# Performance work log

Hardware: AMD Instinct MI355X
Metric: run time of the kernel (lower is better)

The kernel has to match this reference:

```python
import jax, jax.numpy as jnp
import numpy as np

N, S, D_IN, D, H, L, DFF, NRBF = 3072, 256, 64, 256, 8, 3, 1024, 8
LN_EPS = 1e-5
RBF_C = jnp.linspace(0.0, 1.0, NRBF)
RBF_W = jnp.full((NRBF,), 0.15)


def _ln(x, g, b):
    m = x.mean(-1, keepdims=True)
    v = ((x - m) ** 2).mean(-1, keepdims=True)
    return (x - m) * jax.lax.rsqrt(v + LN_EPS) * g + b


def _rbf(v):
    return jnp.exp(-0.5 * ((v[..., None] - RBF_C) / (RBF_W + 1e-6)) ** 2)


def _mha(Q, K, V, Win, bin_, Wout, bout, bias, pad):
    # manual biased MHA: [Lq,D],[Lk,D] -> [Lq,D]; bias [Lq,Lk], pad [Lk] bool
    d = D // H
    q = (Q @ Win[:D].T + bin_[:D]).reshape(-1, H, d).transpose(1, 0, 2)        # [H,Lq,d]
    k = (K @ Win[D:2 * D].T + bin_[D:2 * D]).reshape(-1, H, d).transpose(1, 0, 2)
    v = (V @ Win[2 * D:].T + bin_[2 * D:]).reshape(-1, H, d).transpose(1, 0, 2)
    scores = jnp.einsum('hqd,hkd->hqk', q, k) / (d ** 0.5)
    scores = scores + bias[None]
    scores = scores - 10000.0 * pad.astype(scores.dtype)[None, None, :]
    scores = scores - scores.max(-1, keepdims=True)
    scores = jnp.clip(scores, -20.0, 20.0)
    attn = jax.nn.softmax(scores, axis=-1)
    out = jnp.einsum('hqk,hkd->hqd', attn, v).transpose(1, 0, 2).reshape(-1, D)
    return out @ Wout.T + bout


def _ff(x, W1, b1, W2, b2):
    return jax.nn.gelu(x @ W1.T + b1, approximate=False) @ W2.T + b2


def _forward(x, C, proj_in_W, proj_in_b, pe_W, pe_b, pe_g, pe_beta, pe_gate,
             alpha_nn, beta_sn, sq_W, sq_b,
             sn_Win, sn_bin, sn_Wout, sn_bout, nn_Win, nn_bin, nn_Wout, nn_bout,
             ln_s_g, ln_s_b, ln_n1_g, ln_n1_b, ln_n2_g, ln_n2_b,
             ffn_W1, ffn_b1, ffn_W2, ffn_b2, ffs_W1, ffs_b1, ffs_W2, ffs_b2,
             ln_out_g, ln_out_b, sink_idx, mask_nodes):
    h = x @ proj_in_W.T + proj_in_b                                            # [N,D]
    # correlation-aware node encoding
    Cc = jnp.clip(C, 0.0, 1.0)
    cm, cmax, cmin, cstd = Cc.mean(-1), Cc.max(-1), Cc.min(-1), Cc.std(-1)
    z = jnp.concatenate([cm[:, None], cmax[:, None], cmin[:, None], cstd[:, None],
                         _rbf(cm), _rbf(cmax)], axis=-1)                       # [N,4+2*NRBF]
    pe = pe_gate * _ln(z @ pe_W.T + pe_b, pe_g, pe_beta)
    pe = jnp.where(mask_nodes[:, None], 0.0, pe)
    h = h + pe
    # sink queries (detached gather, then projection)
    sink_q = jax.lax.stop_gradient(h[sink_idx]) @ sq_W.T + sq_b                # [S,D]
    # correlation-derived attention biases
    Cn = C / (jnp.linalg.norm(C, axis=-1, keepdims=True) + 1e-6)
    bias_nn = alpha_nn * (Cn @ Cn.T)                                           # [N,N]
    bias_sn = beta_sn * C.T                                                    # [S,N]
    for l in range(L):
        sq_res = sink_q
        sqn = _ln(sink_q, ln_s_g[l], ln_s_b[l])
        sink_q = sq_res + _mha(sqn, h, h, sn_Win[l], sn_bin[l], sn_Wout[l], sn_bout[l], bias_sn, mask_nodes)
        sink_q = sink_q + _ff(sink_q, ffs_W1[l], ffs_b1[l], ffs_W2[l], ffs_b2[l])
        h_res = h
        hn = _ln(h, ln_n1_g[l], ln_n1_b[l])
        h = h_res + _mha(hn, hn, hn, nn_Win[l], nn_bin[l], nn_Wout[l], nn_bout[l], bias_nn, mask_nodes)
        h = h + _ff(_ln(h, ln_n2_g[l], ln_n2_b[l]), ffn_W1[l], ffn_b1[l], ffn_W2[l], ffn_b2[l])
    return _ln(sink_q, ln_out_g, ln_out_b)                                     # [S,D]


def setup_inputs() -> dict:
    key = jax.random.key(0)
    ks = iter(jax.random.split(key, 48))
    def nrm(shape, s=0.02):
        return jax.random.normal(next(ks), shape, jnp.float32) * s
    FEAT = 4 + 2 * NRBF
    return dict(
        x=jax.random.normal(next(ks), (N, D_IN), jnp.float32),
        C=jax.random.uniform(next(ks), (N, S), jnp.float32),
        sink_idx=jax.random.randint(next(ks), (S,), 0, N),
        mask_nodes=jnp.zeros((N,), bool),
        proj_in_W=nrm((D, D_IN)), proj_in_b=nrm((D,)),
        pe_W=nrm((D, FEAT)), pe_b=nrm((D,)),
        pe_g=jnp.ones((D,)), pe_beta=jnp.zeros((D,)),
        pe_gate=jnp.asarray(0.1, jnp.float32),
        alpha_nn=jnp.asarray(0.3, jnp.float32), beta_sn=jnp.asarray(0.8, jnp.float32),
        sq_W=nrm((D, D)), sq_b=nrm((D,)),
        sn_Win=nrm((L, 3 * D, D)), sn_bin=nrm((L, 3 * D)), sn_Wout=nrm((L, D, D)), sn_bout=nrm((L, D)),
        nn_Win=nrm((L, 3 * D, D)), nn_bin=nrm((L, 3 * D)), nn_Wout=nrm((L, D, D)), nn_bout=nrm((L, D)),
        ln_s_g=jnp.ones((L, D)), ln_s_b=jnp.zeros((L, D)),
        ln_n1_g=jnp.ones((L, D)), ln_n1_b=jnp.zeros((L, D)),
        ln_n2_g=jnp.ones((L, D)), ln_n2_b=jnp.zeros((L, D)),
        ffn_W1=nrm((L, DFF, D)), ffn_b1=nrm((L, DFF)), ffn_W2=nrm((L, D, DFF)), ffn_b2=nrm((L, D)),
        ffs_W1=nrm((L, DFF, D)), ffs_b1=nrm((L, DFF)), ffs_W2=nrm((L, D, DFF)), ffs_b2=nrm((L, D)),
        ln_out_g=jnp.ones((D,)), ln_out_b=jnp.zeros((D,)),
    )


def reference(x, C, sink_idx, mask_nodes, proj_in_W, proj_in_b, pe_W, pe_b, pe_g, pe_beta, pe_gate,
              alpha_nn, beta_sn, sq_W, sq_b,
              sn_Win, sn_bin, sn_Wout, sn_bout, nn_Win, nn_bin, nn_Wout, nn_bout,
              ln_s_g, ln_s_b, ln_n1_g, ln_n1_b, ln_n2_g, ln_n2_b,
              ffn_W1, ffn_b1, ffn_W2, ffn_b2, ffs_W1, ffs_b1, ffs_W2, ffs_b2,
              ln_out_g, ln_out_b):
    return _forward(x, C, proj_in_W, proj_in_b, pe_W, pe_b, pe_g, pe_beta, pe_gate,
                    alpha_nn, beta_sn, sq_W, sq_b,
                    sn_Win, sn_bin, sn_Wout, sn_bout, nn_Win, nn_bin, nn_Wout, nn_bout,
                    ln_s_g, ln_s_b, ln_n1_g, ln_n1_b, ln_n2_g, ln_n2_b,
                    ffn_W1, ffn_b1, ffn_W2, ffn_b2, ffs_W1, ffs_b1, ffs_W2, ffs_b2,
                    ln_out_g, ln_out_b, sink_idx, mask_nodes)
```

## Files before the change

kernel.cpp:

```cpp
#include <hip/hip_runtime.h>
#include <hip/hip_bf16.h>

#define N_NODES 3072
#define S_SINK  256
#define DIN     64
#define NH      8

typedef __attribute__((ext_vector_type(8))) short short8v;
typedef __attribute__((ext_vector_type(4))) float f32x4;

#define LOG2E 1.4426950408889634f

#if defined(__has_builtin)
#if __has_builtin(__builtin_amdgcn_exp2f)
#define EXP2(x) __builtin_amdgcn_exp2f(x)
#else
#define EXP2(x) exp2f(x)
#endif
#else
#define EXP2(x) exp2f(x)
#endif

static __device__ __forceinline__ float gelu_exact(float v) {
    return 0.5f * v * (1.0f + erff(v * 0.70710678118654752f));
}
static __device__ __forceinline__ unsigned short f2b_rne(float f) {
    unsigned int b = __float_as_uint(f);
    b += 0x7fffu + ((b >> 16) & 1u);
    return (unsigned short)(b >> 16);
}
static __device__ __forceinline__ unsigned pack_b16(float a, float b) {
    unsigned r;
    asm("v_cvt_pk_bf16_f32 %0, %1, %2" : "=v"(r) : "v"(a), "v"(b));
    return r;
}
static __device__ __forceinline__ size_t bswz_idx(int m, int n) {
    int qt = m >> 4, cc = m & 15;
    int kt = n >> 4, gg = (n >> 2) & 3, rr = n & 3;
    return (((size_t)qt * 192 + kt) * 64 + gg * 16 + cc) * 4 + rr;
}
static __device__ __forceinline__ size_t kfrag_idx(int h, int k, int d) {
    return (((size_t)(h * 192 + (k >> 4)) * 64) + ((d >> 3) << 4) + (k & 15)) * 8 + (d & 7);
}
static __device__ __forceinline__ size_t vtfrag_idx(int h, int k, int d) {
    return ((((size_t)(h * 48 + (k >> 6)) * 2 + ((k >> 5) & 1)) * 2 + (d >> 4)) * 64
            + ((k >> 3) & 3) * 16 + (d & 15)) * 8 + (k & 7);
}

struct CvtJobs {
    const float* src[9];
    unsigned short* dst[9];
    int cnt4[9];
};
__global__ __launch_bounds__(256) void prep_misc_kernel(CvtJobs cj, int total4, int ncvt,
                                                        const unsigned char* __restrict__ mask,
                                                        float* __restrict__ ma,
                                                        const float* __restrict__ C,
                                                        unsigned short* __restrict__ Cnb)
{
    int b = blockIdx.x;
    if (b < ncvt) {
        int i = b * 256 + threadIdx.x;
        if (i >= total4) return;
        int s = 0, base = 0;
        while (s < 9 && i >= base + cj.cnt4[s]) { base += cj.cnt4[s]; ++s; }
        int off = (i - base) * 4;
        float4 v = *(const float4*)(cj.src[s] + off);
        uint2 o;
        o.x = pack_b16(v.x, v.y);
        o.y = pack_b16(v.z, v.w);
        *(uint2*)(cj.dst[s] + off) = o;
        return;
    }
    b -= ncvt;
    if (b < 12) {
        int j = b * 256 + threadIdx.x;
        if (j < N_NODES) ma[j] = -10000.0f * LOG2E * (float)mask[j];
        return;
    }
    b -= 12;
    int w = threadIdx.x >> 6, lane = threadIdx.x & 63;
    int row = b * 4 + w;
    float4 v = *(const float4*)(C + (size_t)row * 256 + lane * 4);
    float s2 = v.x * v.x + v.y * v.y + v.z * v.z + v.w * v.w;
    #pragma unroll
    for (int o = 32; o > 0; o >>= 1) s2 += __shfl_xor(s2, o);
    float inv = 1.0f / (sqrtf(s2) + 1e-6f);
    uint2 o2;
    o2.x = pack_b16(v.x * inv, v.y * inv);
    o2.y = pack_b16(v.z * inv, v.w * inv);
    *(uint2*)(Cnb + (size_t)row * 256 + lane * 4) = o2;
}

__global__ __launch_bounds__(256) void node_encode_kernel(
    const float* __restrict__ x, const float* __restrict__ C,
    const unsigned char* __restrict__ mask,
    const float* __restrict__ Wp, const float* __restrict__ bp,
    const float* __restrict__ peW, const float* __restrict__ peb,
    const float* __restrict__ peg, const float* __restrict__ pebt,
    const float* __restrict__ gate,
    float* __restrict__ h, unsigned short* __restrict__ hb)
{
    int i = blockIdx.x, t = threadIdx.x;
    __shared__ float xs[DIN];
    __shared__ float r1[256], r2[256];
    __shared__ float zs[20];
    if (t < DIN) xs[t] = x[i * DIN + t];
    float c  = C[i * 256 + t];
    float cc = fminf(fmaxf(c, 0.0f), 1.0f);
    r1[t] = cc; r2[t] = cc * cc;
    __syncthreads();
    for (int s = 128; s > 0; s >>= 1) { if (t < s) { r1[t] += r1[t + s]; r2[t] += r2[t + s]; } __syncthreads(); }
    float cm  = r1[0] * (1.0f / 256.0f);
    float cms = r2[0] * (1.0f / 256.0f);
    __syncthreads();
    r1[t] = cc; r2[t] = cc;
    __syncthreads();
    for (int s = 128; s > 0; s >>= 1) { if (t < s) { r1[t] = fmaxf(r1[t], r1[t + s]); r2[t] = fminf(r2[t], r2[t + s]); } __syncthreads(); }
    float cmax = r1[0], cmin = r2[0];
    __syncthreads();
    if (t == 0) {
        float var  = fmaxf(cms - cm * cm, 0.0f);
        float cstd = sqrtf(var);
        zs[0] = cm; zs[1] = cmax; zs[2] = cmin; zs[3] = cstd;
        float w = 0.15f + 1e-6f;
        for (int k = 0; k < 8; ++k) {
            float ck = (float)k / 7.0f;
            float d1 = (cm   - ck) / w;
            float d2 = (cmax - ck) / w;
            zs[4 + k]  = expf(-0.5f * d1 * d1);
            zs[12 + k] = expf(-0.5f * d2 * d2);
        }
    }
    __syncthreads();
    float pl = peb[t];
    #pragma unroll
    for (int f = 0; f < 20; ++f) pl += zs[f] * peW[t * 20 + f];
    r1[t] = pl; r2[t] = pl * pl;
    __syncthreads();
    for (int s = 128; s > 0; s >>= 1) { if (t < s) { r1[t] += r1[t + s]; r2[t] += r2[t + s]; } __syncthreads(); }
    float m  = r1[0] * (1.0f / 256.0f);
    float vv = fmaxf(r2[0] * (1.0f / 256.0f) - m * m, 0.0f);
    float pe = (pl - m) * rsqrtf(vv + 1e-5f) * peg[t] + pebt[t];
    pe *= gate[0];
    if (mask[i] != 0) pe = 0.0f;
    float hv = bp[t];
    #pragma unroll
    for (int k = 0; k < DIN; ++k) hv += xs[k] * Wp[t * DIN + k];
    float o = hv + pe;
    h[(size_t)i * 256 + t] = o;
    hb[(size_t)i * 256 + t] = f2b_rne(o);
}

static __device__ __forceinline__ void ln_row(const float* in, const float* g, const float* b,
                                              unsigned short* out, int row, int lane) {
    float4 v = *(const float4*)(in + (size_t)row * 256 + lane * 4);
    float s  = v.x + v.y + v.z + v.w;
    float s2 = v.x * v.x + v.y * v.y + v.z * v.z + v.w * v.w;
    #pragma unroll
    for (int o = 32; o > 0; o >>= 1) { s += __shfl_xor(s, o); s2 += __shfl_xor(s2, o); }
    float m  = s * (1.0f / 256.0f);
    float vv = fmaxf(s2 * (1.0f / 256.0f) - m * m, 0.0f);
    float rs = rsqrtf(vv + 1e-5f);
    float4 gg = *(const float4*)(g + lane * 4);
    float4 bb = *(const float4*)(b + lane * 4);
    uint2 o2;
    o2.x = pack_b16((v.x - m) * rs * gg.x + bb.x, (v.y - m) * rs * gg.y + bb.y);
    o2.y = pack_b16((v.z - m) * rs * gg.z + bb.z, (v.w - m) * rs * gg.w + bb.w);
    *(uint2*)(out + (size_t)row * 256 + lane * 4) = o2;
}

__global__ __launch_bounds__(256) void ln_b16_w_kernel(const float* __restrict__ in, const float* __restrict__ g,
                                                       const float* __restrict__ b, unsigned short* __restrict__ out) {
    int w = threadIdx.x >> 6, lane = threadIdx.x & 63;
    ln_row(in, g, b, out, blockIdx.x * 4 + w, lane);
}

__global__ __launch_bounds__(256) void ln_dual_kernel(const float* __restrict__ in0, const float* __restrict__ g0,
                                                      const float* __restrict__ b0, unsigned short* __restrict__ out0, int n0,
                                                      const float* __restrict__ in1, const float* __restrict__ g1,
                                                      const float* __restrict__ b1, unsigned short* __restrict__ out1) {
    int w = threadIdx.x >> 6, lane = threadIdx.x & 63;
    int row = blockIdx.x * 4 + w;
    bool first = row < n0;
    const float* in = first ? in0 : in1;
    const float* g  = first ? g0  : g1;
    const float* b  = first ? b0  : b1;
    unsigned short* out = first ? out0 : out1;
    ln_row(in, g, b, out, first ? row : row - n0, lane);
}

__global__ __launch_bounds__(256) void ln_out_w_kernel(const float* __restrict__ in, const float* __restrict__ g,
                                                       const float* __restrict__ b, float* __restrict__ out) {
    int w = threadIdx.x >> 6, lane = threadIdx.x & 63;
    int row = blockIdx.x * 4 + w;
    float4 v = *(const float4*)(in + (size_t)row * 256 + lane * 4);
    float s  = v.x + v.y + v.z + v.w;
    float s2 = v.x * v.x + v.y * v.y + v.z * v.z + v.w * v.w;
    #pragma unroll
    for (int o = 32; o > 0; o >>= 1) { s += __shfl_xor(s, o); s2 += __shfl_xor(s2, o); }
    float m  = s * (1.0f / 256.0f);
    float vv = fmaxf(s2 * (1.0f / 256.0f) - m * m, 0.0f);
    float rs = rsqrtf(vv + 1e-5f);
    float4 gg = *(const float4*)(g + lane * 4);
    float4 bb = *(const float4*)(b + lane * 4);
    float4 o4;
    o4.x = (v.x - m) * rs * gg.x + bb.x;
    o4.y = (v.y - m) * rs * gg.y + bb.y;
    o4.z = (v.z - m) * rs * gg.z + bb.z;
    o4.w = (v.w - m) * rs * gg.w + bb.w;
    *(float4*)(out + (size_t)row * 256 + lane * 4) = o4;
}

struct GJob {
    const unsigned short* A; const int* ridx; const unsigned short* W;
    const float* bias; const float* res; const float* scale;
    void* out; void* out2; void* vtf;
    int lda, ldw, ldo, omode, kbase, K, act, gx;
    float scmul;
};

static __device__ __forceinline__ void gemm_body(const GJob& j, int bx, int by) {
    __shared__ unsigned short As[64][72];
    __shared__ unsigned short Ws[64][72];
    int tid = threadIdx.x;
    int lane = tid & 63, wid = tid >> 6;
    int c15 = lane & 15, g = lane >> 4;
    int wm = wid & 1, wn = wid >> 1;
    int row0 = by * 64, col0 = bx * 64;
    f32x4 acc[2][2];
    const f32x4 zf = {0.f, 0.f, 0.f, 0.f};
    acc[0][0] = zf; acc[0][1] = zf; acc[1][0] = zf; acc[1][1] = zf;

    for (int k0 = 0; k0 < j.K; k0 += 64) {
        #pragma unroll
        for (int hh = 0; hh < 2; ++hh) {
            int cid = tid + hh * 256;
            int rr = cid >> 3, cc = (cid & 7) * 8;
            int arow = j.ridx ? j.ridx[row0 + rr] : (row0 + rr);
            short8v va = *(const short8v*)(j.A + (size_t)arow * j.lda + k0 + cc);
            short8v vw = *(const short8v*)(j.W + (size_t)(col0 + rr) * j.ldw + k0 + cc);
            *(short8v*)(&As[rr][cc]) = va;
            *(short8v*)(&Ws[rr][cc]) = vw;
        }
        __syncthreads();
        #pragma unroll
        for (int ks = 0; ks < 2; ++ks) {
            short8v a0 = *(const short8v*)(&As[wm * 32 + c15][ks * 32 + g * 8]);
            short8v a1 = *(const short8v*)(&As[wm * 32 + 16 + c15][ks * 32 + g * 8]);
            short8v w0 = *(const short8v*)(&Ws[wn * 32 + c15][ks * 32 + g * 8]);
            short8v w1 = *(const short8v*)(&Ws[wn * 32 + 16 + c15][ks * 32 + g * 8]);
            acc[0][0] = __builtin_amdgcn_mfma_f32_16x16x32_bf16(a0, w0, acc[0][0], 0, 0, 0);
            acc[0][1] = __builtin_amdgcn_mfma_f32_16x16x32_bf16(a0, w1, acc[0][1], 0, 0, 0);
            acc[1][0] = __builtin_amdgcn_mfma_f32_16x16x32_bf16(a1, w0, acc[1][0], 0, 0, 0);
            acc[1][1] = __builtin_amdgcn_mfma_f32_16x16x32_bf16(a1, w1, acc[1][1], 0, 0, 0);
        }
        __syncthreads();
    }
    float sc = (j.scale ? *j.scale : 1.0f) * j.scmul;
    #pragma unroll
    for (int nf = 0; nf < 2; ++nf) {
        int n = col0 + wn * 32 + nf * 16 + c15;
        float bv = j.bias ? j.bias[n] : 0.0f;
        #pragma unroll
        for (int mf = 0; mf < 2; ++mf) {
            #pragma unroll
            for (int r = 0; r < 4; ++r) {
                int m = row0 + wm * 32 + mf * 16 + g * 4 + r;
                float v = acc[mf][nf][r] * sc + bv;
                if (j.act) v = gelu_exact(v);
                if (j.res) v += j.res[(size_t)m * j.ldo + n];
                if (j.omode == 0) {
                    ((float*)j.out)[(size_t)m * j.ldo + n] = v;
                    if (j.out2) ((unsigned short*)j.out2)[(size_t)m * j.ldo + n] = f2b_rne(v);
                } else if (j.omode == 1) {
                    ((unsigned short*)j.out)[(size_t)m * j.ldo + n] = f2b_rne(v);
                } else if (j.omode == 2) {
                    ((unsigned short*)j.out)[bswz_idx(m, n)] = f2b_rne(v);
                } else {
                    unsigned short bw = f2b_rne(v);
                    int nk = n - j.kbase;
                    if (nk < 0) {
                        ((unsigned short*)j.out)[(size_t)m * j.ldo + n] = bw;
                    } else if (nk < 256) {
                        ((unsigned short*)j.out2)[kfrag_idx(nk >> 5, m, nk & 31)] = bw;
                    } else {
                        ((unsigned short*)j.vtf)[vtfrag_idx((nk - 256) >> 5, m, (nk - 256) & 31)] = bw;
                    }
                }
            }
        }
    }
}

__global__ __launch_bounds__(256) void gemm_multi_kernel(GJob j0, GJob j1, GJob j2, int e0, int e1) {
    int b = blockIdx.x;
    GJob j;
    int bb;
    if (b < e0)      { j = j0; bb = b; }
    else if (b < e1) { j = j1; bb = b - e0; }
    else             { j = j2; bb = b - e1; }
    gemm_body(j, bb % j.gx, bb / j.gx);
}

static __device__ __forceinline__ void transpose_body(const float* C, const float* beta,
                                                      const float* maskadd, unsigned short* CTswz,
                                                      int bxi, int byi) {
    __shared__ float tile[32][33];
    int bx = bxi * 32;
    int by = byi * 32;
    int tx = threadIdx.x & 31, ty = threadIdx.x >> 5;
    float bt = beta[0] * LOG2E;
    #pragma unroll
    for (int r = 0; r < 4; ++r) {
        int row = bx + ty + r * 8;
        tile[ty + r * 8][tx] = C[(size_t)row * 256 + by + tx];
    }
    __syncthreads();
    #pragma unroll
    for (int r = 0; r < 4; ++r) {
        int srow = by + ty + r * 8;
        int col  = bx + tx;
        CTswz[bswz_idx(srow, col)] = f2b_rne(bt * tile[tx][ty + r * 8] + maskadd[col]);
    }
}

__global__ __launch_bounds__(256) void mega0_kernel(
    const float* __restrict__ C, const float* __restrict__ beta,
    const float* __restrict__ maskadd, unsigned short* __restrict__ CTswz,
    GJob j0, GJob j1, int ntr, int e0)
{
    int b = blockIdx.x;
    if (b < ntr) { transpose_body(C, beta, maskadd, CTswz, b % 96, b / 96); return; }
    b -= ntr;
    GJob j;
    int bb;
    if (b < e0) { j = j0; bb = b; }
    else        { j = j1; bb = b - e0; }
    gemm_body(j, bb % j.gx, bb / j.gx);
}

template<int SPLIT>
static __device__ __forceinline__ void attn_body(
    const unsigned short* __restrict__ Qb, int ldq,
    const unsigned short* __restrict__ Kfrag,
    const unsigned short* __restrict__ VTfrag,
    const unsigned short* __restrict__ biasswz,
    unsigned short* __restrict__ out, int qx)
{
    constexpr int KT = 48 / SPLIT;
    __shared__ unsigned short P_all[SPLIT * 32 * 72];
    __shared__ float ml[SPLIT * 64];
    const int head = blockIdx.y;
    const int i0 = qx * 32;
    const int qt0 = qx * 2;
    const int tid = threadIdx.x;
    const int lane = tid & 63, w = tid >> 6;
    const int c15 = lane & 15, g = lane >> 4;
    unsigned short* P_lds = P_all + w * (32 * 72);
    const unsigned short* Kf  = Kfrag  + (size_t)head * 192 * 512;
    const unsigned short* VTf = VTfrag + (size_t)head * 48 * 2048;
    const f32x4 zf = {0.f, 0.f, 0.f, 0.f};
    const float rsl2 = 0.25503164113124427f;

    short8v qf[2];
    #pragma unroll
    for (int nf = 0; nf < 2; ++nf)
        qf[nf] = *(const short8v*)(Qb + (size_t)(i0 + nf * 16 + c15) * ldq + head * 32 + g * 8);

    float m_[2] = {-1e30f, -1e30f};
    float l_[2] = {0.f, 0.f};
    f32x4 acc[2][2];
    acc[0][0] = zf; acc[0][1] = zf; acc[1][0] = zf; acc[1][1] = zf;

    for (int kt = 0; kt < KT; ++kt) {
        const int k0 = (w * KT + kt) * 64;
        const int kt16 = k0 >> 4;
        short8v kf[4];
        #pragma unroll
        for (int mf = 0; mf < 4; ++mf)
            kf[mf] = *(const short8v*)(Kf + ((size_t)(kt16 + mf) * 64 + lane) * 8);
        f32x4 s[4][2];
        __builtin_amdgcn_s_setprio(1);
        #pragma unroll
        for (int mf = 0; mf < 4; ++mf)
            #pragma unroll
            for (int nf = 0; nf < 2; ++nf)
                s[mf][nf] = __builtin_amdgcn_mfma_f32_16x16x32_bf16(kf[mf], qf[nf], zf, 0, 0, 0);
        __builtin_amdgcn_s_setprio(0);
        #pragma unroll
        for (int nf = 0; nf < 2; ++nf) {
            const unsigned short* bb = biasswz + ((size_t)(qt0 + nf) * 192 + kt16) * 256 + lane * 4;
            #pragma unroll
            for (int mf = 0; mf < 4; ++mf) {
                uint2 bv = *(const uint2*)(bb + mf * 256);
                s[mf][nf][0] = s[mf][nf][0] * rsl2 + __uint_as_float(bv.x << 16);
                s[mf][nf][1] = s[mf][nf][1] * rsl2 + __uint_as_float(bv.x & 0xffff0000u);
                s[mf][nf][2] = s[mf][nf][2] * rsl2 + __uint_as_float(bv.y << 16);
                s[mf][nf][3] = s[mf][nf][3] * rsl2 + __uint_as_float(bv.y & 0xffff0000u);
            }
        }
        #pragma unroll
        for (int nf = 0; nf < 2; ++nf) {
            float t0 = fmaxf(fmaxf(s[0][nf][0], s[0][nf][1]), fmaxf(s[0][nf][2], s[0][nf][3]));
            float t1 = fmaxf(fmaxf(s[1][nf][0], s[1][nf][1]), fmaxf(s[1][nf][2], s[1][nf][3]));
            float t2 = fmaxf(fmaxf(s[2][nf][0], s[2][nf][1]), fmaxf(s[2][nf][2], s[2][nf][3]));
            float t3 = fmaxf(fmaxf(s[3][nf][0], s[3][nf][1]), fmaxf(s[3][nf][2], s[3][nf][3]));
            float tmax = fmaxf(fmaxf(t0, t1), fmaxf(t2, t3));
            tmax = fmaxf(tmax, __shfl_xor(tmax, 16));
            tmax = fmaxf(tmax, __shfl_xor(tmax, 32));
            if (!__all(tmax <= m_[nf] + 8.0f)) {
                float mn = fmaxf(m_[nf], tmax);
                float scl = EXP2(m_[nf] - mn);
                m_[nf] = mn;
                l_[nf] *= scl;
                #pragma unroll
                for (int mf = 0; mf < 2; ++mf) {
                    acc[mf][nf][0] *= scl; acc[mf][nf][1] *= scl;
                    acc[mf][nf][2] *= scl; acc[mf][nf][3] *= scl;
                }
            }
            float mcur = m_[nf];
            float ps0 = 0.f, ps1 = 0.f, ps2 = 0.f, ps3 = 0.f;
            #pragma unroll
            for (int mf = 0; mf < 4; ++mf) {
                float p0 = EXP2(s[mf][nf][0] - mcur);
                float p1 = EXP2(s[mf][nf][1] - mcur);
                float p2 = EXP2(s[mf][nf][2] - mcur);
                float p3 = EXP2(s[mf][nf][3] - mcur);
                s[mf][nf][0] = p0; s[mf][nf][1] = p1;
                s[mf][nf][2] = p2; s[mf][nf][3] = p3;
                ps0 += p0; ps1 += p1; ps2 += p2; ps3 += p3;
            }
            l_[nf] += (ps0 + ps1) + (ps2 + ps3);
            const int q = nf * 16 + c15;
            #pragma unroll
            for (int mf = 0; mf < 4; ++mf) {
                uint2 pv;
                pv.x = pack_b16(s[mf][nf][0], s[mf][nf][1]);
                pv.y = pack_b16(s[mf][nf][2], s[mf][nf][3]);
                *(uint2*)(P_lds + q * 72 + mf * 16 + g * 4) = pv;
            }
        }
        const unsigned short* vb = VTf + (size_t)(k0 >> 6) * 2048;
        #pragma unroll
        for (int ks = 0; ks < 2; ++ks) {
            short8v pB[2], vA[2];
            #pragma unroll
            for (int nf = 0; nf < 2; ++nf)
                pB[nf] = *(const short8v*)(P_lds + (nf * 16 + c15) * 72 + ks * 32 + g * 8);
            #pragma unroll
            for (int mf = 0; mf < 2; ++mf)
                vA[mf] = *(const short8v*)(vb + ((size_t)(ks * 2 + mf) * 64 + lane) * 8);
            __builtin_amdgcn_s_setprio(1);
            #pragma unroll
            for (int mf = 0; mf < 2; ++mf)
                #pragma unroll
                for (int nf = 0; nf < 2; ++nf)
                    acc[mf][nf] = __builtin_amdgcn_mfma_f32_16x16x32_bf16(vA[mf], pB[nf], acc[mf][nf], 0, 0, 0);
            __builtin_amdgcn_s_setprio(0);
        }
    }

    float* Olds = (float*)P_all;
    #pragma unroll
    for (int nf = 0; nf < 2; ++nf) {
        float lv = l_[nf];
        lv += __shfl_xor(lv, 16);
        lv += __shfl_xor(lv, 32);
        int q = nf * 16 + c15;
        #pragma unroll
        for (int mf = 0; mf < 2; ++mf)
            *(f32x4*)(Olds + w * 1152 + q * 36 + mf * 16 + g * 4) = acc[mf][nf];
        if (g == 0) {
            ml[w * 64 + q] = m_[nf];
            ml[w * 64 + 32 + q] = lv;
        }
    }
    __syncthreads();
    if (tid < 256) {
        int q = tid >> 3, d0 = (tid & 7) * 4;
        float M = -1e30f;
        #pragma unroll
        for (int s = 0; s < SPLIT; ++s) M = fmaxf(M, ml[s * 64 + q]);
        float L = 0.f;
        float v0 = 0, v1 = 0, v2 = 0, v3 = 0;
        #pragma unroll
        for (int s = 0; s < SPLIT; ++s) {
            float wv = EXP2(ml[s * 64 + q] - M);
            L += wv * ml[s * 64 + 32 + q];
            const float* op = Olds + s * 1152 + q * 36 + d0;
            v0 += wv * op[0]; v1 += wv * op[1];
            v2 += wv * op[2]; v3 += wv * op[3];
        }
        float invL = 1.0f / L;
        uint2 pk;
        pk.x = pack_b16(v0 * invL, v1 * invL);
        pk.y = pack_b16(v2 * invL, v3 * invL);
        *(uint2*)(out + (size_t)(i0 + q) * 256 + head * 32 + d0) = pk;
    }
}

template<int SPLIT>
__global__ __launch_bounds__(64 * SPLIT) void attn_multi_kernel(
    const unsigned short* Q0, const unsigned short* K0, const unsigned short* V0,
    const unsigned short* B0, unsigned short* O0, int nx0,
    const unsigned short* Q1, const unsigned short* K1, const unsigned short* V1,
    const unsigned short* B1, unsigned short* O1)
{
    int bx = blockIdx.x;
    bool first = bx < nx0;
    const unsigned short* Q = first ? Q0 : Q1;
    const unsigned short* K = first ? K0 : K1;
    const unsigned short* V = first ? V0 : V1;
    const unsigned short* B = first ? B0 : B1;
    unsigned short* O = first ? O0 : O1;
    attn_body<SPLIT>(Q, 256, K, V, B, O, first ? bx : bx - nx0);
}

extern "C" void kernel_launch(void* const* d_in, const int* in_sizes, int n_in,
                              void* d_out, int out_size, void* d_ws, size_t ws_size,
                              hipStream_t stream)
{
    const float* x        = (const float*)d_in[0];
    const float* C        = (const float*)d_in[1];
    const int*   sidx     = (const int*)d_in[2];
    const unsigned char* mask = (const unsigned char*)d_in[3];
    const float* proj_W   = (const float*)d_in[4];
    const float* proj_b   = (const float*)d_in[5];
    const float* peW      = (const float*)d_in[6];
    const float* peb      = (const float*)d_in[7];
    const float* peg      = (const float*)d_in[8];
    const float* pebt     = (const float*)d_in[9];
    const float* pe_gate  = (const float*)d_in[10];
    const float* alpha_nn = (const float*)d_in[11];
    const float* beta_sn  = (const float*)d_in[12];
    const float* sqW      = (const float*)d_in[13];
    const float* sqb      = (const float*)d_in[14];
    const float* sn_Win   = (const float*)d_in[15];
    const float* sn_bin   = (const float*)d_in[16];
    const float* sn_Wout  = (const float*)d_in[17];
    const float* sn_bout  = (const float*)d_in[18];
    const float* nn_Win   = (const float*)d_in[19];
    const float* nn_bin   = (const float*)d_in[20];
    const float* nn_Wout  = (const float*)d_in[21];
    const float* nn_bout  = (const float*)d_in[22];
    const float* ln_s_g   = (const float*)d_in[23];
    const float* ln_s_b   = (const float*)d_in[24];
    const float* ln_n1_g  = (const float*)d_in[25];
    const float* ln_n1_b  = (const float*)d_in[26];
    const float* ln_n2_g  = (const float*)d_in[27];
    const float* ln_n2_b  = (const float*)d_in[28];
    const float* ffn_W1   = (const float*)d_in[29];
    const float* ffn_b1   = (const float*)d_in[30];
    const float* ffn_W2   = (const float*)d_in[31];
    const float* ffn_b2   = (const float*)d_in[32];
    const float* ffs_W1   = (const float*)d_in[33];
    const float* ffs_b1   = (const float*)d_in[34];
    const float* ffs_W2   = (const float*)d_in[35];
    const float* ffs_b2   = (const float*)d_in[36];
    const float* ln_og    = (const float*)d_in[37];
    const float* ln_ob    = (const float*)d_in[38];

    float* ws = (float*)d_ws;
    float* h       = ws;
    float* sinkq   = ws + 786432;
    float* maskadd = ws + 851968;
    unsigned short* Cnb     = (unsigned short*)(ws + 856064);
    unsigned short* hb      = (unsigned short*)(ws + 1249280);
    unsigned short* hnb     = (unsigned short*)(ws + 1642496);
    unsigned short* attnob_n= (unsigned short*)(ws + 2035712);
    unsigned short* attnob_s= (unsigned short*)(ws + 2428928);
    unsigned short* sqnb    = (unsigned short*)(ws + 2461696);
    unsigned short* sinkqb  = (unsigned short*)(ws + 2494464);
    unsigned short* Kfrag_n = (unsigned short*)(ws + 2527232);
    unsigned short* VTfrag_n= (unsigned short*)(ws + 2920448);
    unsigned short* Kfrag_s = (unsigned short*)(ws + 3313664);
    unsigned short* VTfrag_s= (unsigned short*)(ws + 3706880);
    unsigned short* CTswz   = (unsigned short*)(ws + 4100096);
    unsigned short* biasswz = (unsigned short*)(ws + 4493312);
    unsigned short* wb      = (unsigned short*)(ws + 9211904);
    float* big      = ws + 11603968;
    unsigned short* sqWb    = wb;
    unsigned short* snWinb  = wb + 65536;
    unsigned short* snWoutb = wb + 655360;
    unsigned short* nnWinb  = wb + 851968;
    unsigned short* nnWoutb = wb + 1441792;
    unsigned short* ffnW1b  = wb + 1638400;
    unsigned short* ffnW2b  = wb + 2424832;
    unsigned short* ffsW1b  = wb + 3211264;
    unsigned short* ffsW2b  = wb + 3997696;
    unsigned short* q_sb  = (unsigned short*)big;
    unsigned short* mid_sb= (unsigned short*)big + 65536;
    unsigned short* Qnb   = (unsigned short*)big + 327680;
    unsigned short* midb  = (unsigned short*)big + 1114112;

    dim3 b256(256), b512(512);
    GJob jz = {};  jz.gx = 1;

    CvtJobs cj;
    cj.src[0] = sqW;     cj.dst[0] = sqWb;    cj.cnt4[0] = 16384;
    cj.src[1] = sn_Win;  cj.dst[1] = snWinb;  cj.cnt4[1] = 147456;
    cj.src[2] = sn_Wout; cj.dst[2] = snWoutb; cj.cnt4[2] = 49152;
    cj.src[3] = nn_Win;  cj.dst[3] = nnWinb;  cj.cnt4[3] = 147456;
    cj.src[4] = nn_Wout; cj.dst[4] = nnWoutb; cj.cnt4[4] = 49152;
    cj.src[5] = ffn_W1;  cj.dst[5] = ffnW1b;  cj.cnt4[5] = 196608;
    cj.src[6] = ffn_W2;  cj.dst[6] = ffnW2b;  cj.cnt4[6] = 196608;
    cj.src[7] = ffs_W1;  cj.dst[7] = ffsW1b;  cj.cnt4[7] = 196608;
    cj.src[8] = ffs_W2;  cj.dst[8] = ffsW2b;  cj.cnt4[8] = 196608;

    prep_misc_kernel<<<4672 + 12 + 768, b256, 0, stream>>>(cj, 1196032, 4672, mask, maskadd, C, Cnb);
    node_encode_kernel<<<N_NODES, b256, 0, stream>>>(x, C, mask, proj_W, proj_b, peW, peb, peg, pebt, pe_gate, h, hb);
    {
        GJob j0 = {hb, sidx, sqWb, sqb, nullptr, nullptr, sinkq, nullptr, nullptr, 256, 256, 256, 0, 0, 256, 0, 4, 1.0f};
        GJob j1 = {Cnb, nullptr, Cnb, maskadd, nullptr, alpha_nn, biasswz, nullptr, nullptr, 256, 256, 3072, 2, 0, 256, 0, 48, LOG2E};
        mega0_kernel<<<768 + 16 + 2304, b256, 0, stream>>>(C, beta_sn, maskadd, CTswz, j0, j1, 768, 16);
    }

    for (int l = 0; l < 3; ++l) {
        const float* lsg = ln_s_g + l * 256,  *lsb = ln_s_b + l * 256;
        const float* l1g = ln_n1_g + l * 256, *l1b = ln_n1_b + l * 256;
        ln_dual_kernel<<<832, b256, 0, stream>>>(sinkq, lsg, lsb, sqnb, 256, h, l1g, l1b, hnb);
        {
            GJob j0 = {sqnb, nullptr, snWinb + (size_t)l * 196608, sn_bin + l * 768, nullptr, nullptr, q_sb, nullptr, nullptr, 256, 256, 256, 1, 0, 256, 0, 4, 1.0f};
            GJob j1 = {hb, nullptr, snWinb + (size_t)l * 196608 + 65536, sn_bin + l * 768 + 256, nullptr, nullptr, nullptr, Kfrag_s, VTfrag_s, 256, 256, 0, 3, 0, 256, 0, 8, 1.0f};
            GJob j2 = {hnb, nullptr, nnWinb + (size_t)l * 196608, nn_bin + l * 768, nullptr, nullptr, Qnb, Kfrag_n, VTfrag_n, 256, 256, 256, 3, 256, 256, 0, 12, 1.0f};
            gemm_multi_kernel<<<16 + 384 + 576, b256, 0, stream>>>(j0, j1, j2, 16, 16 + 384);
        }
        attn_multi_kernel<8><<<dim3(8 + 96, 8), b512, 0, stream>>>(
            q_sb, Kfrag_s, VTfrag_s, CTswz, attnob_s, 8,
            Qnb, Kfrag_n, VTfrag_n, biasswz, attnob_n);
        {
            GJob j0 = {attnob_s, nullptr, snWoutb + (size_t)l * 65536, sn_bout + l * 256, sinkq, nullptr, sinkq, sinkqb, nullptr, 256, 256, 256, 0, 0, 256, 0, 4, 1.0f};
            GJob j1 = {attnob_n, nullptr, nnWoutb + (size_t)l * 65536, nn_bout + l * 256, h, nullptr, h, nullptr, nullptr, 256, 256, 256, 0, 0, 256, 0, 4, 1.0f};
            gemm_multi_kernel<<<16 + 192, b256, 0, stream>>>(j0, j1, jz, 16, 16 + 192);
        }
        ln_b16_w_kernel<<<768, b256, 0, stream>>>(h, ln_n2_g + l * 256, ln_n2_b + l * 256, hnb);
        {
            GJob j0 = {sinkqb, nullptr, ffsW1b + (size_t)l * 262144, ffs_b1 + l * 1024, nullptr, nullptr, mid_sb, nullptr, nullptr, 256, 256, 1024, 1, 0, 256, 1, 16, 1.0f};
            GJob j1 = {hnb, nullptr, ffnW1b + (size_t)l * 262144, ffn_b1 + l * 1024, nullptr, nullptr, midb, nullptr, nullptr, 256, 256, 1024, 1, 0, 256, 1, 16, 1.0f};
            gemm_multi_kernel<<<64 + 768, b256, 0, stream>>>(j0, j1, jz, 64, 64 + 768);
        }
        {
            GJob j0 = {mid_sb, nullptr, ffsW2b + (size_t)l * 262144, ffs_b2 + l * 256, sinkq, nullptr, sinkq, nullptr, nullptr, 1024, 1024, 256, 0, 0, 1024, 0, 4, 1.0f};
            GJob j1 = {midb, nullptr, ffnW2b + (size_t)l * 262144, ffn_b2 + l * 256, h, nullptr, h, hb, nullptr, 1024, 1024, 256, 0, 0, 1024, 0, 4, 1.0f};
            gemm_multi_kernel<<<16 + 192, b256, 0, stream>>>(j0, j1, jz, 16, 16 + 192);
        }
    }

    ln_out_w_kernel<<<64, b256, 0, stream>>>(sinkq, ln_og, ln_ob, (float*)d_out);
}
```

Measured before the change: 341.2 us.

## Fuse LayerNorm into GEMM A-tile load, drop standalone LN kernels

Removes the separate ln_dual and ln_b16 kernels. The GEMM now takes the fp32 pre-norm activations plus gamma and beta. Each block first computes per-row mean and rstd into shared memory, then normalizes and converts to bf16 while staging the A tile. This saves two kernel launches per layer and the bf16 normalized-activation round trip through memory. In exchange, every column tile recomputes the row statistics and reads fp32 A, which is twice the bytes of bf16, across all N-tiles (12 or 16 column blocks).

Result: slower. 440.7 us (+29.1%).

```diff
diff --git a/kernel.cpp b/kernel.cpp
--- a/kernel.cpp
+++ b/kernel.cpp
@@ -152,44 +152,6 @@
     hb[(size_t)i * 256 + t] = f2b_rne(o);
 }
 
-static __device__ __forceinline__ void ln_row(const float* in, const float* g, const float* b,
-                                              unsigned short* out, int row, int lane) {
-    float4 v = *(const float4*)(in + (size_t)row * 256 + lane * 4);
-    float s  = v.x + v.y + v.z + v.w;
-    float s2 = v.x * v.x + v.y * v.y + v.z * v.z + v.w * v.w;
-    #pragma unroll
-    for (int o = 32; o > 0; o >>= 1) { s += __shfl_xor(s, o); s2 += __shfl_xor(s2, o); }
-    float m  = s * (1.0f / 256.0f);
-    float vv = fmaxf(s2 * (1.0f / 256.0f) - m * m, 0.0f);
-    float rs = rsqrtf(vv + 1e-5f);
-    float4 gg = *(const float4*)(g + lane * 4);
-    float4 bb = *(const float4*)(b + lane * 4);
-    uint2 o2;
-    o2.x = pack_b16((v.x - m) * rs * gg.x + bb.x, (v.y - m) * rs * gg.y + bb.y);
-    o2.y = pack_b16((v.z - m) * rs * gg.z + bb.z, (v.w - m) * rs * gg.w + bb.w);
-    *(uint2*)(out + (size_t)row * 256 + lane * 4) = o2;
-}
-
-__global__ __launch_bounds__(256) void ln_b16_w_kernel(const float* __restrict__ in, const float* __restrict__ g,
-                                                       const float* __restrict__ b, unsigned short* __restrict__ out) {
-    int w = threadIdx.x >> 6, lane = threadIdx.x & 63;
-    ln_row(in, g, b, out, blockIdx.x * 4 + w, lane);
-}
-
-__global__ __launch_bounds__(256) void ln_dual_kernel(const float* __restrict__ in0, const float* __restrict__ g0,
-                                                      const float* __restrict__ b0, unsigned short* __restrict__ out0, int n0,
-                                                      const float* __restrict__ in1, const float* __restrict__ g1,
-                                                      const float* __restrict__ b1, unsigned short* __restrict__ out1) {
-    int w = threadIdx.x >> 6, lane = threadIdx.x & 63;
-    int row = blockIdx.x * 4 + w;
-    bool first = row < n0;
-    const float* in = first ? in0 : in1;
-    const float* g  = first ? g0  : g1;
-    const float* b  = first ? b0  : b1;
-    unsigned short* out = first ? out0 : out1;
-    ln_row(in, g, b, out, first ? row : row - n0, lane);
-}
-
 __global__ __launch_bounds__(256) void ln_out_w_kernel(const float* __restrict__ in, const float* __restrict__ g,
                                                        const float* __restrict__ b, float* __restrict__ out) {
     int w = threadIdx.x >> 6, lane = threadIdx.x & 63;
@@ -216,6 +178,7 @@
     const unsigned short* A; const int* ridx; const unsigned short* W;
     const float* bias; const float* res; const float* scale;
     void* out; void* out2; void* vtf;
+    const float* lnA; const float* lng; const float* lnb;
     int lda, ldw, ldo, omode, kbase, K, act, gx;
     float scmul;
 };
@@ -223,6 +186,7 @@
 static __device__ __forceinline__ void gemm_body(const GJob& j, int bx, int by) {
     __shared__ unsigned short As[64][72];
     __shared__ unsigned short Ws[64][72];
+    __shared__ float lnm[64], lnr[64];
     int tid = threadIdx.x;
     int lane = tid & 63, wid = tid >> 6;
     int c15 = lane & 15, g = lane >> 4;
@@ -232,16 +196,54 @@
     const f32x4 zf = {0.f, 0.f, 0.f, 0.f};
     acc[0][0] = zf; acc[0][1] = zf; acc[1][0] = zf; acc[1][1] = zf;
 
+    if (j.lnA) {
+        int r = tid >> 2, p = tid & 3;
+        int arow = j.ridx ? j.ridx[row0 + r] : (row0 + r);
+        const float* src = j.lnA + (size_t)arow * j.lda + p * 64;
+        float s = 0.f, s2 = 0.f;
+        #pragma unroll
+        for (int i = 0; i < 16; ++i) {
+            float4 v = *(const float4*)(src + i * 4);
+            s  += (v.x + v.y) + (v.z + v.w);
+            s2 += (v.x * v.x + v.y * v.y) + (v.z * v.z + v.w * v.w);
+        }
+        s  += __shfl_xor(s, 1);  s2 += __shfl_xor(s2, 1);
+        s  += __shfl_xor(s, 2);  s2 += __shfl_xor(s2, 2);
+        if (p == 0) {
+            float m = s * (1.0f / 256.0f);
+            float vv = fmaxf(s2 * (1.0f / 256.0f) - m * m, 0.0f);
+            lnm[r] = m;
+            lnr[r] = rsqrtf(vv + 1e-5f);
+        }
+        __syncthreads();
+    }
+
     for (int k0 = 0; k0 < j.K; k0 += 64) {
         #pragma unroll
         for (int hh = 0; hh < 2; ++hh) {
             int cid = tid + hh * 256;
             int rr = cid >> 3, cc = (cid & 7) * 8;
             int arow = j.ridx ? j.ridx[row0 + rr] : (row0 + rr);
-            short8v va = *(const short8v*)(j.A + (size_t)arow * j.lda + k0 + cc);
-            short8v vw = *(const short8v*)(j.W + (size_t)(col0 + rr) * j.ldw + k0 + cc);
-            *(short8v*)(&As[rr][cc]) = va;
-            *(short8v*)(&Ws[rr][cc]) = vw;
+            if (j.lnA) {
+                const float* p4 = j.lnA + (size_t)arow * j.lda + k0 + cc;
+                float m = lnm[rr], rs = lnr[rr];
+                float4 a0 = *(const float4*)p4;
+                float4 a1 = *(const float4*)(p4 + 4);
+                float4 g0 = *(const float4*)(j.lng + k0 + cc);
+                float4 g1 = *(const float4*)(j.lng + k0 + cc + 4);
+                float4 b0 = *(const float4*)(j.lnb + k0 + cc);
+                float4 b1 = *(const float4*)(j.lnb + k0 + cc + 4);
+                uint2 lo, hi;
+                lo.x = pack_b16((a0.x - m) * rs * g0.x + b0.x, (a0.y - m) * rs * g0.y + b0.y);
+                lo.y = pack_b16((a0.z - m) * rs * g0.z + b0.z, (a0.w - m) * rs * g0.w + b0.w);
+                hi.x = pack_b16((a1.x - m) * rs * g1.x + b1.x, (a1.y - m) * rs * g1.y + b1.y);
+                hi.y = pack_b16((a1.z - m) * rs * g1.z + b1.z, (a1.w - m) * rs * g1.w + b1.w);
+                *(uint2*)(&As[rr][cc]) = lo;
+                *(uint2*)(&As[rr][cc + 4]) = hi;
+            } else {
+                *(short8v*)(&As[rr][cc]) = *(const short8v*)(j.A + (size_t)arow * j.lda + k0 + cc);
+            }
+            *(short8v*)(&Ws[rr][cc]) = *(const short8v*)(j.W + (size_t)(col0 + rr) * j.ldw + k0 + cc);
         }
         __syncthreads();
         #pragma unroll
@@ -568,10 +570,8 @@
     float* maskadd = ws + 851968;
     unsigned short* Cnb     = (unsigned short*)(ws + 856064);
     unsigned short* hb      = (unsigned short*)(ws + 1249280);
-    unsigned short* hnb     = (unsigned short*)(ws + 1642496);
     unsigned short* attnob_n= (unsigned short*)(ws + 2035712);
     unsigned short* attnob_s= (unsigned short*)(ws + 2428928);
-    unsigned short* sqnb    = (unsigned short*)(ws + 2461696);
     unsigned short* sinkqb  = (unsigned short*)(ws + 2494464);
     unsigned short* Kfrag_n = (unsigned short*)(ws + 2527232);
     unsigned short* VTfrag_n= (unsigned short*)(ws + 2920448);
@@ -612,38 +612,48 @@
     prep_misc_kernel<<<4672 + 12 + 768, b256, 0, stream>>>(cj, 1196032, 4672, mask, maskadd, C, Cnb);
     node_encode_kernel<<<N_NODES, b256, 0, stream>>>(x, C, mask, proj_W, proj_b, peW, peb, peg, pebt, pe_gate, h, hb);
     {
-        GJob j0 = {hb, sidx, sqWb, sqb, nullptr, nullptr, sinkq, nullptr, nullptr, 256, 256, 256, 0, 0, 256, 0, 4, 1.0f};
-        GJob j1 = {Cnb, nullptr, Cnb, maskadd, nullptr, alpha_nn, biasswz, nullptr, nullptr, 256, 256, 3072, 2, 0, 256, 0, 48, LOG2E};
+        GJob j0 = {hb, sidx, sqWb, sqb, nullptr, nullptr, sinkq, nullptr, nullptr,
+                   nullptr, nullptr, nullptr, 256, 256, 256, 0, 0, 256, 0, 4, 1.0f};
+        GJob j1 = {Cnb, nullptr, Cnb, maskadd, nullptr, alpha_nn, biasswz, nullptr, nullptr,
+                   nullptr, nullptr, nullptr, 256, 256, 3072, 2, 0, 256, 0, 48, LOG2E};
         mega0_kernel<<<768 + 16 + 2304, b256, 0, stream>>>(C, beta_sn, maskadd, CTswz, j0, j1, 768, 16);
     }
 
     for (int l = 0; l < 3; ++l) {
         const float* lsg = ln_s_g + l * 256,  *lsb = ln_s_b + l * 256;
         const float* l1g = ln_n1_g + l * 256, *l1b = ln_n1_b + l * 256;
-        ln_dual_kernel<<<832, b256, 0, stream>>>(sinkq, lsg, lsb, sqnb, 256, h, l1g, l1b, hnb);
+        const float* l2g = ln_n2_g + l * 256, *l2b = ln_n2_b + l * 256;
         {
-            GJob j0 = {sqnb, nullptr, snWinb + (size_t)l * 196608, sn_bin + l * 768, nullptr, nullptr, q_sb, nullptr, nullptr, 256, 256, 256, 1, 0, 256, 0, 4, 1.0f};
-            GJob j1 = {hb, nullptr, snWinb + (size_t)l * 196608 + 65536, sn_bin + l * 768 + 256, nullptr, nullptr, nullptr, Kfrag_s, VTfrag_s, 256, 256, 0, 3, 0, 256, 0, 8, 1.0f};
-            GJob j2 = {hnb, nullptr, nnWinb + (size_t)l * 196608, nn_bin + l * 768, nullptr, nullptr, Qnb, Kfrag_n, VTfrag_n, 256, 256, 256, 3, 256, 256, 0, 12, 1.0f};
+            GJob j0 = {nullptr, nullptr, snWinb + (size_t)l * 196608, sn_bin + l * 768, nullptr, nullptr,
+                       q_sb, nullptr, nullptr, sinkq, lsg, lsb, 256, 256, 256, 1, 0, 256, 0, 4, 1.0f};
+            GJob j1 = {hb, nullptr, snWinb + (size_t)l * 196608 + 65536, sn_bin + l * 768 + 256, nullptr, nullptr,
+                       nullptr, Kfrag_s, VTfrag_s, nullptr, nullptr, nullptr, 256, 256, 0, 3, 0, 256, 0, 8, 1.0f};
+            GJob j2 = {nullptr, nullptr, nnWinb + (size_t)l * 196608, nn_bin + l * 768, nullptr, nullptr,
+                       Qnb, Kfrag_n, VTfrag_n, h, l1g, l1b, 256, 256, 256, 3, 256, 256, 0, 12, 1.0f};
             gemm_multi_kernel<<<16 + 384 + 576, b256, 0, stream>>>(j0, j1, j2, 16, 16 + 384);
         }
         attn_multi_kernel<8><<<dim3(8 + 96, 8), b512, 0, stream>>>(
             q_sb, Kfrag_s, VTfrag_s, CTswz, attnob_s, 8,
             Qnb, Kfrag_n, VTfrag_n, biasswz, attnob_n);
         {
-            GJob j0 = {attnob_s, nullptr, snWoutb + (size_t)l * 65536, sn_bout + l * 256, sinkq, nullptr, sinkq, sinkqb, nullptr, 256, 256, 256, 0, 0, 256, 0, 4, 1.0f};
-            GJob j1 = {attnob_n, nullptr, nnWoutb + (size_t)l * 65536, nn_bout + l * 256, h, nullptr, h, nullptr, nullptr, 256, 256, 256, 0, 0, 256, 0, 4, 1.0f};
+            GJob j0 = {attnob_s, nullptr, snWoutb + (size_t)l * 65536, sn_bout + l * 256, sinkq, nullptr,
+                       sinkq, sinkqb, nullptr, nullptr, nullptr, nullptr, 256, 256, 256, 0, 0, 256, 0, 4, 1.0f};
+            GJob j1 = {attnob_n, nullptr, nnWoutb + (size_t)l * 65536, nn_bout + l * 256, h, nullptr,
+                       h, nullptr, nullptr, nullptr, nullptr, nullptr, 256, 256, 256, 0, 0, 256, 0, 4, 1.0f};
             gemm_multi_kernel<<<16 + 192, b256, 0, stream>>>(j0, j1, jz, 16, 16 + 192);
         }
-        ln_b16_w_kernel<<<768, b256, 0, stream>>>(h, ln_n2_g + l * 256, ln_n2_b + l * 256, hnb);
         {
-            GJob j0 = {sinkqb, nullptr, ffsW1b + (size_t)l * 262144, ffs_b1 + l * 1024, nullptr, nullptr, mid_sb, nullptr, nullptr, 256, 256, 1024, 1, 0, 256, 1, 16, 1.0f};
-            GJob j1 = {hnb, nullptr, ffnW1b + (size_t)l * 262144, ffn_b1 + l * 1024, nullptr, nullptr, midb, nullptr, nullptr, 256, 256, 1024, 1, 0, 256, 1, 16, 1.0f};
+            GJob j0 = {sinkqb, nullptr, ffsW1b + (size_t)l * 262144, ffs_b1 + l * 1024, nullptr, nullptr,
+                       mid_sb, nullptr, nullptr, nullptr, nullptr, nullptr, 256, 256, 1024, 1, 0, 256, 1, 16, 1.0f};
+            GJob j1 = {nullptr, nullptr, ffnW1b + (size_t)l * 262144, ffn_b1 + l * 1024, nullptr, nullptr,
+                       midb, nullptr, nullptr, h, l2g, l2b, 256, 256, 1024, 1, 0, 256, 1, 16, 1.0f};
             gemm_multi_kernel<<<64 + 768, b256, 0, stream>>>(j0, j1, jz, 64, 64 + 768);
         }
         {
-            GJob j0 = {mid_sb, nullptr, ffsW2b + (size_t)l * 262144, ffs_b2 + l * 256, sinkq, nullptr, sinkq, nullptr, nullptr, 1024, 1024, 256, 0, 0, 1024, 0, 4, 1.0f};
-            GJob j1 = {midb, nullptr, ffnW2b + (size_t)l * 262144, ffn_b2 + l * 256, h, nullptr, h, hb, nullptr, 1024, 1024, 256, 0, 0, 1024, 0, 4, 1.0f};
+            GJob j0 = {mid_sb, nullptr, ffsW2b + (size_t)l * 262144, ffs_b2 + l * 256, sinkq, nullptr,
+                       sinkq, nullptr, nullptr, nullptr, nullptr, nullptr, 1024, 1024, 256, 0, 0, 1024, 0, 4, 1.0f};
+            GJob j1 = {midb, nullptr, ffnW2b + (size_t)l * 262144, ffn_b2 + l * 256, h, nullptr,
+                       h, hb, nullptr, nullptr, nullptr, nullptr, 1024, 1024, 256, 0, 0, 1024, 0, 4, 1.0f};
             gemm_multi_kernel<<<16 + 192, b256, 0, stream>>>(j0, j1, jz, 16, 16 + 192);
         }
     }
```
